# Optimization experiments

Measured on AMD Instinct MI355X. Metric: run time of the kernel, lower is better.

The kernel has to match this reference:

```python
import math
import jax, jax.numpy as jnp
import numpy as np

N_HEADS, INPUT_DIM, EMBED_DIM = 8, 512, 512
KEY_DIM = EMBED_DIM // N_HEADS  # 64, val_dim == key_dim
BATCH, N = 4, 2048


def setup_inputs() -> dict:
    key = jax.random.key(0)
    ks = jax.random.split(key, 6)
    def unif(k, shape):
        stdv = 1.0 / math.sqrt(shape[-1])
        return jax.random.uniform(k, shape, jnp.float32, -stdv, stdv)
    q = jax.random.normal(ks[0], (BATCH, N, INPUT_DIM), jnp.float32)
    mask = jax.random.randint(ks[1], (BATCH, N, N), 0, 2, jnp.int32)
    W_query = unif(ks[2], (N_HEADS, INPUT_DIM, KEY_DIM))
    W_key = unif(ks[3], (N_HEADS, INPUT_DIM, KEY_DIM))
    W_val = unif(ks[4], (N_HEADS, INPUT_DIM, KEY_DIM))
    W_out = unif(ks[5], (N_HEADS, KEY_DIM, EMBED_DIM))
    return {"q": q, "mask": mask, "W_query": W_query, "W_key": W_key,
            "W_val": W_val, "W_out": W_out}


def reference(q, mask, W_query, W_key, W_val, W_out):
    # Self-attention: k is None, v is None -> k = q, v = q (module forward_).
    norm = 1.0 / math.sqrt(KEY_DIM)
    m = mask.astype(bool)[None]  # (1, b, nq, ng) broadcast over heads
    Q = jnp.einsum('bnd,hdk->hbnk', q, W_query)  # (h, b, nq, dk)
    K = jnp.einsum('bnd,hdk->hbnk', q, W_key)    # (h, b, ng, dk)
    V = jnp.einsum('bnd,hdv->hbnv', q, W_val)    # (h, b, ng, dv)
    scores = norm * jnp.einsum('hbqk,hbgk->hbqg', Q, K)  # (h, b, nq, ng)
    scores = jnp.where(m, -jnp.inf, scores)
    attn = jax.nn.softmax(scores, axis=-1)
    attn = jnp.where(m, 0.0, attn)  # zero out masked (also kills NaN rows)
    heads = jnp.einsum('hbqg,hbgv->hbqv', attn, V)
    out = jnp.einsum('hbqv,hve->bqe', heads, W_out)  # (b, nq, embed)
    return out
```

## Files before the change

### kernel.cpp

```cpp
#include <hip/hip_runtime.h>
#include <hip/hip_bf16.h>
#include <stdint.h>

using bf16 = __hip_bfloat16;
typedef __attribute__((ext_vector_type(8))) short short8;
typedef __attribute__((ext_vector_type(4))) short short4b;
typedef __attribute__((ext_vector_type(4))) float f32x4;
typedef __attribute__((ext_vector_type(4))) unsigned int u32x4;

#if __has_builtin(__builtin_amdgcn_exp2f)
#define EXP2(x) __builtin_amdgcn_exp2f(x)
#else
#define EXP2(x) exp2f(x)
#endif

__device__ __forceinline__ short8 load8(const bf16* p) {
  return *reinterpret_cast<const short8*>(p);
}
__device__ __forceinline__ short f2b(float f) {
  return __builtin_bit_cast(short, __float2bfloat16(f));
}
__device__ __forceinline__ unsigned int pk2(float a, float b) {
  return (unsigned int)(unsigned short)f2b(a) |
         ((unsigned int)(unsigned short)f2b(b) << 16);
}
__device__ __forceinline__ void asy16(const bf16* g, bf16* l) {
  __builtin_amdgcn_global_load_lds(
      (const __attribute__((address_space(1))) void*)g,
      (__attribute__((address_space(3))) void*)l, 16, 0, 0);
}


__global__ void k_prep(const float4* __restrict__ x, ushort4* __restrict__ xb,
                       const float* __restrict__ Wq, const float* __restrict__ Wk,
                       const float* __restrict__ Wv, const float* __restrict__ Wo,
                       bf16* __restrict__ Wcat, bf16* __restrict__ Wot,
                       const int4* __restrict__ m4,
                       unsigned long long* __restrict__ bits) {
  int blk = blockIdx.x;
  const int tid = threadIdx.x;
  if (blk < 4096) {
    int i = blk * 256 + tid;
    float4 v = x[i];
    ushort4 o;
    o.x = (unsigned short)f2b(v.x);
    o.y = (unsigned short)f2b(v.y);
    o.z = (unsigned short)f2b(v.z);
    o.w = (unsigned short)f2b(v.w);
    xb[i] = o;
  } else if (blk < 4352) {
    int t = blk - 4096;
    __shared__ float T[64][65];
    if (t < 192) {
      int which = t >> 6;
      int h = (t >> 3) & 7, dt = t & 7;
      const float* W = (which == 0) ? Wq : ((which == 1) ? Wk : Wv);
#pragma unroll
      for (int p = 0; p < 4; ++p) {
        int row = p * 16 + (tid >> 4);
        float4 v = *(const float4*)(W + (size_t)(h * 512 + dt * 64 + row) * 64 +
                                    (tid & 15) * 4);
        T[row][(tid & 15) * 4 + 0] = v.x;
        T[row][(tid & 15) * 4 + 1] = v.y;
        T[row][(tid & 15) * 4 + 2] = v.z;
        T[row][(tid & 15) * 4 + 3] = v.w;
      }
      __syncthreads();
      float scale = (which == 0) ? 0.18033688011112042f : 1.0f;
      int jj = tid >> 2, i0 = (tid & 3) * 16;
#pragma unroll
      for (int q = 0; q < 2; ++q) {
        short8 o;
#pragma unroll
        for (int e = 0; e < 8; ++e) o[e] = f2b(T[i0 + q * 8 + e][jj] * scale);
        *(short8*)(Wcat + (size_t)(which * 512 + h * 64 + jj) * 512 + dt * 64 +
                   i0 + q * 8) = o;
      }
    } else {
      int t2 = t - 192;
      int h = t2 >> 3, et = t2 & 7;
#pragma unroll
      for (int p = 0; p < 4; ++p) {
        int row = p * 16 + (tid >> 4);
        float4 v = *(const float4*)(Wo + (size_t)(h * 64 + row) * 512 + et * 64 +
                                    (tid & 15) * 4);
        T[row][(tid & 15) * 4 + 0] = v.x;
        T[row][(tid & 15) * 4 + 1] = v.y;
        T[row][(tid & 15) * 4 + 2] = v.z;
        T[row][(tid & 15) * 4 + 3] = v.w;
      }
      __syncthreads();
      int jj = tid >> 2, i0 = (tid & 3) * 16;
#pragma unroll
      for (int q = 0; q < 2; ++q) {
        short8 o;
#pragma unroll
        for (int e = 0; e < 8; ++e) o[e] = f2b(T[i0 + q * 8 + e][jj]);
        *(short8*)(Wot + (size_t)(et * 64 + jj) * 512 + h * 64 + i0 + q * 8) = o;
      }
    }
  } else {
    int i = (blk - 4352) * 256 + tid;
    int4 v = m4[i];
    unsigned int nib = (unsigned)(v.x != 0) | ((unsigned)(v.y != 0) << 1) |
                       ((unsigned)(v.z != 0) << 2) | ((unsigned)(v.w != 0) << 3);
    unsigned long long w = (unsigned long long)nib << (4 * (tid & 15));
    w |= __shfl_xor(w, 1);
    w |= __shfl_xor(w, 2);
    w |= __shfl_xor(w, 4);
    w |= __shfl_xor(w, 8);
    if ((tid & 15) == 0) bits[i >> 4] = w;
  }
}

__device__ __forceinline__ void gemm128(const bf16* __restrict__ A,
                                        const bf16* __restrict__ Bt,
                                        bf16* As, bf16* Bs,
                                        int rowBase, int colBase,
                                        f32x4 acc[4][4]) {
  const int tid = threadIdx.x;
  const int lane = tid & 63, w = tid >> 6;
  const int g = lane >> 4, r = lane & 15;

  auto stage = [&](int buf, int s) {
#pragma unroll
    for (int p = 0; p < 2; ++p) {
      int c = p * 256 + tid;
      int row = c >> 2, gr = c & 3, sg = gr ^ (row & 3);
      asy16(A + (size_t)(rowBase + row) * 512 + s * 32 + sg * 8,
            As + buf * 4096 + c * 8);
    }
#pragma unroll
    for (int p = 0; p < 2; ++p) {
      int c = p * 256 + tid;
      int row = c >> 2, gr = c & 3, sg = gr ^ (row & 3);
      asy16(Bt + (size_t)(colBase + row) * 512 + s * 32 + sg * 8,
            Bs + buf * 4096 + c * 8);
    }
  };

  stage(0, 0);
  int buf = 0;
  const int rbl = (w >> 1) * 64, cbl = (w & 1) * 64;
  for (int s = 0; s < 16; ++s) {
    __syncthreads();
    if (s < 15) stage(buf ^ 1, s + 1);
    const bf16* a0 = As + buf * 4096;
    const bf16* b0 = Bs + buf * 4096;
    short8 af[4], bfr[4];
#pragma unroll
    for (int mt = 0; mt < 4; ++mt) {
      int row = rbl + mt * 16 + r;
      af[mt] = load8(a0 + (row * 4 + (g ^ (row & 3))) * 8);
    }
#pragma unroll
    for (int nt = 0; nt < 4; ++nt) {
      int col = cbl + nt * 16 + r;
      bfr[nt] = load8(b0 + (col * 4 + (g ^ (col & 3))) * 8);
    }
#pragma unroll
    for (int mt = 0; mt < 4; ++mt)
#pragma unroll
      for (int nt = 0; nt < 4; ++nt)
        acc[mt][nt] = __builtin_amdgcn_mfma_f32_16x16x32_bf16(
            af[mt], bfr[nt], acc[mt][nt], 0, 0, 0);
    buf ^= 1;
  }
}

__global__ __launch_bounds__(256, 3) void k_proj_qkv(
    const bf16* __restrict__ Xb, const bf16* __restrict__ Wcat,
    bf16* __restrict__ Qb, bf16* __restrict__ Kp, bf16* __restrict__ Vp) {
  __shared__ __align__(16) bf16 As[2 * 4096];
  __shared__ __align__(16) bf16 Bs[2 * 4096];
  int rowBase = blockIdx.x * 128, colBase = blockIdx.y * 128;
  f32x4 acc[4][4] = {};
  gemm128(Xb, Wcat, As, Bs, rowBase, colBase, acc);
  const int lane = threadIdx.x & 63, w = threadIdx.x >> 6;
  const int g = lane >> 4, r = lane & 15;
#pragma unroll
  for (int mt = 0; mt < 4; ++mt) {
    int row0 = rowBase + (w >> 1) * 64 + mt * 16 + 4 * g;
    int b = row0 >> 11, n0 = row0 & 2047;
    int kt = n0 >> 6;
#pragma unroll
    for (int nt = 0; nt < 4; ++nt) {
      int col = colBase + (w & 1) * 64 + nt * 16 + r;
      if (col < 512) {
        int hh = col >> 6, dk = col & 63;
        bf16* p0 = Qb + ((size_t)(b * 8 + hh) * 2048 + n0) * 64 + dk;
#pragma unroll
        for (int rr = 0; rr < 4; ++rr)
          p0[rr * 64] = __float2bfloat16(acc[mt][nt][rr]);
      } else if (col < 1024) {
        int hh = (col >> 6) & 7, dk = col & 63;
        int half = dk >> 5, gk = (dk >> 3) & 3, jj = dk & 7;
        int kr = n0 & 63;
        int kc = kr >> 4, r0 = kr & 15;
        bf16* base = Kp + (size_t)(b * 8 + hh) * 131072 + (size_t)kt * 4096 +
                     ((kc * 2 + half) * 4 + gk) * 128 + jj;
#pragma unroll
        for (int rr = 0; rr < 4; ++rr)
          base[(r0 + rr) * 8] = __float2bfloat16(acc[mt][nt][rr]);
      } else {
        int hdv = col - 1024;
        int hh = hdv >> 6, dv = hdv & 63;
        int dvs = dv >> 4, rv = dv & 15;
        int kcol0 = n0 & 63;
        int half = kcol0 >> 5, gv = (kcol0 >> 2) & 3;
        int j0 = ((kcol0 >> 4) & 1) * 4;
        short4b pkv;
#pragma unroll
        for (int rr = 0; rr < 4; ++rr) pkv[rr] = f2b(acc[mt][nt][rr]);
        *reinterpret_cast<short4b*>(
            Vp + (size_t)(b * 8 + hh) * 131072 + (size_t)kt * 4096 +
            (((half * 4 + dvs) * 4 + gv) * 16 + rv) * 8 + j0) = pkv;
      }
    }
  }
}

__global__ __launch_bounds__(256, 2) void k_proj_out(
    const bf16* __restrict__ O, const bf16* __restrict__ Wot,
    float* __restrict__ out) {
  __shared__ __align__(16) bf16 As[2 * 4096];
  __shared__ __align__(16) bf16 Bs[2 * 4096];
  int rowBase = blockIdx.x * 128, colBase = blockIdx.y * 128;
  f32x4 acc[4][4] = {};
  gemm128(O, Wot, As, Bs, rowBase, colBase, acc);
  const int lane = threadIdx.x & 63, w = threadIdx.x >> 6;
  const int g = lane >> 4, r = lane & 15;
#pragma unroll
  for (int mt = 0; mt < 4; ++mt) {
    int row0 = rowBase + (w >> 1) * 64 + mt * 16 + 4 * g;
#pragma unroll
    for (int nt = 0; nt < 4; ++nt) {
      int col = colBase + (w & 1) * 64 + nt * 16 + r;
#pragma unroll
      for (int rr = 0; rr < 4; ++rr)
        out[(size_t)(row0 + rr) * 512 + col] = acc[mt][nt][rr];
    }
  }
}

__global__ __launch_bounds__(256, 2) void k_attn(const bf16* __restrict__ Q,
    const bf16* __restrict__ K, const bf16* __restrict__ V,
    const unsigned long long* __restrict__ MB, bf16* __restrict__ O) {
  const int blin = blockIdx.x;
  const int j = blin >> 3;
  const int bh = (blin & 7) * 4 + (j >> 4);
  const int qt = j & 15;
  const int b = bh >> 3, h = bh & 7;
  const int tid = threadIdx.x;
  const int lane = tid & 63;
  const int wave = tid >> 6;
  const int g = lane >> 4, r = lane & 15;
  const int qbase = qt * 128 + wave * 32;

  __shared__ __align__(16) bf16 Kl[3][4096];
  __shared__ __align__(16) bf16 Vl[3][4096];

  const bf16* Kp = K + (size_t)bh * 131072;
  const bf16* Vp = V + (size_t)bh * 131072;

  short8 qf[2][2];
#pragma unroll
  for (int s = 0; s < 2; ++s) {
    const bf16* Qp = Q + ((size_t)bh * 2048 + qbase + s * 16 + r) * 64;
    qf[s][0] = load8(Qp + g * 8);
    qf[s][1] = load8(Qp + 32 + g * 8);
  }
  const unsigned long long* Mp0 = MB + ((size_t)b * 2048 + qbase + r) * 32;
  const unsigned long long* Mp1 = MB + ((size_t)b * 2048 + qbase + 16 + r) * 32;

  short8 ones;
#pragma unroll
  for (int i = 0; i < 8; ++i) ones[i] = (short)0x3F80;

  f32x4 acc[2][4] = {};
  f32x4 acc_l[2] = {};

  auto stage = [&](int buf, int kt) {
    const bf16* Kg = Kp + (size_t)kt * 4096;
    const bf16* Vg = Vp + (size_t)kt * 4096;
#pragma unroll
    for (int p = 0; p < 2; ++p) {
      int c = p * 256 + tid;
      asy16(Kg + c * 8, &Kl[buf][0] + c * 8);
    }
#pragma unroll
    for (int p = 0; p < 2; ++p) {
      int c = p * 256 + tid;
      asy16(Vg + c * 8, &Vl[buf][0] + c * 8);
    }
  };

  auto qk = [&](const bf16* kl, f32x4 stl[4][2]) {
#pragma unroll
    for (int kc = 0; kc < 4; ++kc) {
      short8 kf0 = load8(kl + ((kc * 2 + 0) * 4 + g) * 128 + r * 8);
      short8 kf1 = load8(kl + ((kc * 2 + 1) * 4 + g) * 128 + r * 8);
      f32x4 z0 = {};
      z0 = __builtin_amdgcn_mfma_f32_16x16x32_bf16(kf0, qf[0][0], z0, 0, 0, 0);
      stl[kc][0] = __builtin_amdgcn_mfma_f32_16x16x32_bf16(kf1, qf[0][1], z0, 0, 0, 0);
      f32x4 z1 = {};
      z1 = __builtin_amdgcn_mfma_f32_16x16x32_bf16(kf0, qf[1][0], z1, 0, 0, 0);
      stl[kc][1] = __builtin_amdgcn_mfma_f32_16x16x32_bf16(kf1, qf[1][1], z1, 0, 0, 0);
    }
  };

  stage(0, 0);
  stage(1, 1);
  unsigned long long mw0c = Mp0[0], mw1c = Mp1[0];
  __syncthreads();
  f32x4 st_cur[4][2];
  qk(&Kl[0][0], st_cur);

  int b_cur = 0, b_nxt = 1, b_st = 2;

  for (int kt = 0; kt < 32; ++kt) {
    __syncthreads();
    if (kt < 30) stage(b_st, kt + 2);
    unsigned long long mw0n = 0, mw1n = 0;
    if (kt < 31) { mw0n = Mp0[kt + 1]; mw1n = Mp1[kt + 1]; }

    f32x4 stn[4][2];
    if (kt < 31) qk(&Kl[b_nxt][0], stn);

    short8 pa[2][2];
#pragma unroll
    for (int s = 0; s < 2; ++s) {
      unsigned long long mw = s ? mw1c : mw0c;
      unsigned ml = (unsigned)mw >> (4 * g);
      unsigned mh = (unsigned)(mw >> 32) >> (4 * g);
      float p[16];
#pragma unroll
      for (int kc = 0; kc < 4; ++kc)
#pragma unroll
        for (int rr = 0; rr < 4; ++rr) {
          float e = EXP2(st_cur[kc][s][rr]);
          unsigned wsel = (kc & 2) ? mh : ml;
          bool bad = (wsel >> (((kc & 1) << 4) + rr)) & 1u;
          p[kc * 4 + rr] = bad ? 0.f : e;
        }
      u32x4 q0, q1;
#pragma unroll
      for (int i2 = 0; i2 < 4; ++i2) {
        q0[i2] = pk2(p[2 * i2], p[2 * i2 + 1]);
        q1[i2] = pk2(p[8 + 2 * i2], p[8 + 2 * i2 + 1]);
      }
      pa[s][0] = __builtin_bit_cast(short8, q0);
      pa[s][1] = __builtin_bit_cast(short8, q1);
      acc_l[s] = __builtin_amdgcn_mfma_f32_16x16x32_bf16(pa[s][0], ones, acc_l[s], 0, 0, 0);
      acc_l[s] = __builtin_amdgcn_mfma_f32_16x16x32_bf16(pa[s][1], ones, acc_l[s], 0, 0, 0);
    }

    const bf16* vl = &Vl[b_cur][0];
#pragma unroll
    for (int dvs = 0; dvs < 4; ++dvs) {
      short8 vb0 = load8(vl + ((0 * 4 + dvs) * 4 + g) * 128 + r * 8);
      short8 vb1 = load8(vl + ((1 * 4 + dvs) * 4 + g) * 128 + r * 8);
#pragma unroll
      for (int s = 0; s < 2; ++s) {
        acc[s][dvs] = __builtin_amdgcn_mfma_f32_16x16x32_bf16(pa[s][0], vb0, acc[s][dvs], 0, 0, 0);
        acc[s][dvs] = __builtin_amdgcn_mfma_f32_16x16x32_bf16(pa[s][1], vb1, acc[s][dvs], 0, 0, 0);
      }
    }

#pragma unroll
    for (int kc = 0; kc < 4; ++kc) {
      st_cur[kc][0] = stn[kc][0];
      st_cur[kc][1] = stn[kc][1];
    }
    mw0c = mw0n;
    mw1c = mw1n;
    int t = b_cur; b_cur = b_nxt; b_nxt = b_st; b_st = t;
  }

#pragma unroll
  for (int s = 0; s < 2; ++s) {
    float inv[4];
#pragma unroll
    for (int rr = 0; rr < 4; ++rr)
      inv[rr] = (acc_l[s][rr] > 0.f) ? 1.f / acc_l[s][rr] : 0.f;
    bf16* Op = O + ((size_t)b * 2048 + qbase + s * 16 + 4 * g) * 512 + h * 64;
#pragma unroll
    for (int dvs = 0; dvs < 4; ++dvs)
#pragma unroll
      for (int rr = 0; rr < 4; ++rr)
        Op[rr * 512 + dvs * 16 + r] = __float2bfloat16(acc[s][dvs][rr] * inv[rr]);
  }
}


extern "C" void kernel_launch(void* const* d_in, const int* in_sizes, int n_in,
                              void* d_out, int out_size, void* d_ws, size_t ws_size,
                              hipStream_t stream) {
  const float* q    = (const float*)d_in[0];
  const int*   mask = (const int*)d_in[1];
  const float* Wq   = (const float*)d_in[2];
  const float* Wk   = (const float*)d_in[3];
  const float* Wv   = (const float*)d_in[4];
  const float* Wo   = (const float*)d_in[5];
  float* out = (float*)d_out;

  char* ws = (char*)d_ws;
  const size_t MB1 = 1024 * 1024;
  bf16* Xb   = (bf16*)(ws + 0);
  bf16* Qb   = (bf16*)(ws + 8 * MB1);
  bf16* Kpm  = (bf16*)(ws + 16 * MB1);
  bf16* Vpm  = (bf16*)(ws + 24 * MB1);
  bf16* Ob   = (bf16*)(ws + 32 * MB1);
  unsigned long long* Mbits = (unsigned long long*)(ws + 40 * MB1);
  bf16* Wcat = (bf16*)(ws + 42 * MB1);
  bf16* Wot  = (bf16*)(ws + 42 * MB1 + 1536 * 512 * 2);

  k_prep<<<20736, 256, 0, stream>>>((const float4*)q, (ushort4*)Xb,
                                    Wq, Wk, Wv, Wo, Wcat, Wot,
                                    (const int4*)mask, Mbits);
  k_proj_qkv<<<dim3(64, 12), 256, 0, stream>>>(Xb, Wcat, Qb, Kpm, Vpm);
  k_attn<<<512, 256, 0, stream>>>(Qb, Kpm, Vpm, Mbits, Ob);
  k_proj_out<<<dim3(64, 4), 256, 0, stream>>>(Ob, Wot, out);
}
```

Before: 214.5 us.

## Use 8 waves of 16 query rows per attention block instead of 4x32

```diff
diff --git a/kernel.cpp b/kernel.cpp
--- a/kernel.cpp
+++ b/kernel.cpp
@@ -243,7 +243,7 @@
   }
 }
 
-__global__ __launch_bounds__(256, 2) void k_attn(const bf16* __restrict__ Q,
+__global__ __launch_bounds__(512, 4) void k_attn(const bf16* __restrict__ Q,
     const bf16* __restrict__ K, const bf16* __restrict__ V,
     const unsigned long long* __restrict__ MB, bf16* __restrict__ O) {
   const int blin = blockIdx.x;
@@ -255,7 +255,7 @@
   const int lane = tid & 63;
   const int wave = tid >> 6;
   const int g = lane >> 4, r = lane & 15;
-  const int qbase = qt * 128 + wave * 32;
+  const int qbase = qt * 128 + wave * 16;
 
   __shared__ __align__(16) bf16 Kl[3][4096];
   __shared__ __align__(16) bf16 Vl[3][4096];
@@ -263,57 +263,44 @@
   const bf16* Kp = K + (size_t)bh * 131072;
   const bf16* Vp = V + (size_t)bh * 131072;
 
-  short8 qf[2][2];
-#pragma unroll
-  for (int s = 0; s < 2; ++s) {
-    const bf16* Qp = Q + ((size_t)bh * 2048 + qbase + s * 16 + r) * 64;
-    qf[s][0] = load8(Qp + g * 8);
-    qf[s][1] = load8(Qp + 32 + g * 8);
-  }
-  const unsigned long long* Mp0 = MB + ((size_t)b * 2048 + qbase + r) * 32;
-  const unsigned long long* Mp1 = MB + ((size_t)b * 2048 + qbase + 16 + r) * 32;
+  short8 qf0, qf1;
+  {
+    const bf16* Qp = Q + ((size_t)bh * 2048 + qbase + r) * 64;
+    qf0 = load8(Qp + g * 8);
+    qf1 = load8(Qp + 32 + g * 8);
+  }
+  const unsigned long long* Mp = MB + ((size_t)b * 2048 + qbase + r) * 32;
 
   short8 ones;
 #pragma unroll
   for (int i = 0; i < 8; ++i) ones[i] = (short)0x3F80;
 
-  f32x4 acc[2][4] = {};
-  f32x4 acc_l[2] = {};
+  f32x4 acc[4] = {};
+  f32x4 acc_l = {};
 
   auto stage = [&](int buf, int kt) {
     const bf16* Kg = Kp + (size_t)kt * 4096;
     const bf16* Vg = Vp + (size_t)kt * 4096;
-#pragma unroll
-    for (int p = 0; p < 2; ++p) {
-      int c = p * 256 + tid;
-      asy16(Kg + c * 8, &Kl[buf][0] + c * 8);
-    }
-#pragma unroll
-    for (int p = 0; p < 2; ++p) {
-      int c = p * 256 + tid;
-      asy16(Vg + c * 8, &Vl[buf][0] + c * 8);
-    }
+    asy16(Kg + tid * 8, &Kl[buf][0] + tid * 8);
+    asy16(Vg + tid * 8, &Vl[buf][0] + tid * 8);
   };
 
-  auto qk = [&](const bf16* kl, f32x4 stl[4][2]) {
+  auto qk = [&](const bf16* kl, f32x4 stl[4]) {
 #pragma unroll
     for (int kc = 0; kc < 4; ++kc) {
       short8 kf0 = load8(kl + ((kc * 2 + 0) * 4 + g) * 128 + r * 8);
       short8 kf1 = load8(kl + ((kc * 2 + 1) * 4 + g) * 128 + r * 8);
-      f32x4 z0 = {};
-      z0 = __builtin_amdgcn_mfma_f32_16x16x32_bf16(kf0, qf[0][0], z0, 0, 0, 0);
-      stl[kc][0] = __builtin_amdgcn_mfma_f32_16x16x32_bf16(kf1, qf[0][1], z0, 0, 0, 0);
-      f32x4 z1 = {};
-      z1 = __builtin_amdgcn_mfma_f32_16x16x32_bf16(kf0, qf[1][0], z1, 0, 0, 0);
-      stl[kc][1] = __builtin_amdgcn_mfma_f32_16x16x32_bf16(kf1, qf[1][1], z1, 0, 0, 0);
+      f32x4 z = {};
+      z = __builtin_amdgcn_mfma_f32_16x16x32_bf16(kf0, qf0, z, 0, 0, 0);
+      stl[kc] = __builtin_amdgcn_mfma_f32_16x16x32_bf16(kf1, qf1, z, 0, 0, 0);
     }
   };
 
   stage(0, 0);
   stage(1, 1);
-  unsigned long long mw0c = Mp0[0], mw1c = Mp1[0];
+  unsigned long long mwc = Mp[0];
   __syncthreads();
-  f32x4 st_cur[4][2];
+  f32x4 st_cur[4];
   qk(&Kl[0][0], st_cur);
 
   int b_cur = 0, b_nxt = 1, b_st = 2;
@@ -321,75 +308,60 @@
   for (int kt = 0; kt < 32; ++kt) {
     __syncthreads();
     if (kt < 30) stage(b_st, kt + 2);
-    unsigned long long mw0n = 0, mw1n = 0;
-    if (kt < 31) { mw0n = Mp0[kt + 1]; mw1n = Mp1[kt + 1]; }
-
-    f32x4 stn[4][2];
+    unsigned long long mwn = 0;
+    if (kt < 31) mwn = Mp[kt + 1];
+
+    f32x4 stn[4];
     if (kt < 31) qk(&Kl[b_nxt][0], stn);
 
-    short8 pa[2][2];
-#pragma unroll
-    for (int s = 0; s < 2; ++s) {
-      unsigned long long mw = s ? mw1c : mw0c;
-      unsigned ml = (unsigned)mw >> (4 * g);
-      unsigned mh = (unsigned)(mw >> 32) >> (4 * g);
-      float p[16];
-#pragma unroll
-      for (int kc = 0; kc < 4; ++kc)
-#pragma unroll
-        for (int rr = 0; rr < 4; ++rr) {
-          float e = EXP2(st_cur[kc][s][rr]);
-          unsigned wsel = (kc & 2) ? mh : ml;
-          bool bad = (wsel >> (((kc & 1) << 4) + rr)) & 1u;
-          p[kc * 4 + rr] = bad ? 0.f : e;
-        }
-      u32x4 q0, q1;
-#pragma unroll
-      for (int i2 = 0; i2 < 4; ++i2) {
-        q0[i2] = pk2(p[2 * i2], p[2 * i2 + 1]);
-        q1[i2] = pk2(p[8 + 2 * i2], p[8 + 2 * i2 + 1]);
-      }
-      pa[s][0] = __builtin_bit_cast(short8, q0);
-      pa[s][1] = __builtin_bit_cast(short8, q1);
-      acc_l[s] = __builtin_amdgcn_mfma_f32_16x16x32_bf16(pa[s][0], ones, acc_l[s], 0, 0, 0);
-      acc_l[s] = __builtin_amdgcn_mfma_f32_16x16x32_bf16(pa[s][1], ones, acc_l[s], 0, 0, 0);
-    }
+    unsigned ml = (unsigned)mwc >> (4 * g);
+    unsigned mh = (unsigned)(mwc >> 32) >> (4 * g);
+    float p[16];
+#pragma unroll
+    for (int kc = 0; kc < 4; ++kc)
+#pragma unroll
+      for (int rr = 0; rr < 4; ++rr) {
+        float e = EXP2(st_cur[kc][rr]);
+        unsigned wsel = (kc & 2) ? mh : ml;
+        bool bad = (wsel >> (((kc & 1) << 4) + rr)) & 1u;
+        p[kc * 4 + rr] = bad ? 0.f : e;
+      }
+    u32x4 q0, q1;
+#pragma unroll
+    for (int i2 = 0; i2 < 4; ++i2) {
+      q0[i2] = pk2(p[2 * i2], p[2 * i2 + 1]);
+      q1[i2] = pk2(p[8 + 2 * i2], p[8 + 2 * i2 + 1]);
+    }
+    short8 pa0 = __builtin_bit_cast(short8, q0);
+    short8 pa1 = __builtin_bit_cast(short8, q1);
+    acc_l = __builtin_amdgcn_mfma_f32_16x16x32_bf16(pa0, ones, acc_l, 0, 0, 0);
+    acc_l = __builtin_amdgcn_mfma_f32_16x16x32_bf16(pa1, ones, acc_l, 0, 0, 0);
 
     const bf16* vl = &Vl[b_cur][0];
 #pragma unroll
     for (int dvs = 0; dvs < 4; ++dvs) {
       short8 vb0 = load8(vl + ((0 * 4 + dvs) * 4 + g) * 128 + r * 8);
       short8 vb1 = load8(vl + ((1 * 4 + dvs) * 4 + g) * 128 + r * 8);
-#pragma unroll
-      for (int s = 0; s < 2; ++s) {
-        acc[s][dvs] = __builtin_amdgcn_mfma_f32_16x16x32_bf16(pa[s][0], vb0, acc[s][dvs], 0, 0, 0);
-        acc[s][dvs] = __builtin_amdgcn_mfma_f32_16x16x32_bf16(pa[s][1], vb1, acc[s][dvs], 0, 0, 0);
-      }
-    }
-
-#pragma unroll
-    for (int kc = 0; kc < 4; ++kc) {
-      st_cur[kc][0] = stn[kc][0];
-      st_cur[kc][1] = stn[kc][1];
-    }
-    mw0c = mw0n;
-    mw1c = mw1n;
+      acc[dvs] = __builtin_amdgcn_mfma_f32_16x16x32_bf16(pa0, vb0, acc[dvs], 0, 0, 0);
+      acc[dvs] = __builtin_amdgcn_mfma_f32_16x16x32_bf16(pa1, vb1, acc[dvs], 0, 0, 0);
+    }
+
+#pragma unroll
+    for (int kc = 0; kc < 4; ++kc) st_cur[kc] = stn[kc];
+    mwc = mwn;
     int t = b_cur; b_cur = b_nxt; b_nxt = b_st; b_st = t;
   }
 
-#pragma unroll
-  for (int s = 0; s < 2; ++s) {
-    float inv[4];
+  float inv[4];
+#pragma unroll
+  for (int rr = 0; rr < 4; ++rr)
+    inv[rr] = (acc_l[rr] > 0.f) ? 1.f / acc_l[rr] : 0.f;
+  bf16* Op = O + ((size_t)b * 2048 + qbase + 4 * g) * 512 + h * 64;
+#pragma unroll
+  for (int dvs = 0; dvs < 4; ++dvs)
 #pragma unroll
     for (int rr = 0; rr < 4; ++rr)
-      inv[rr] = (acc_l[s][rr] > 0.f) ? 1.f / acc_l[s][rr] : 0.f;
-    bf16* Op = O + ((size_t)b * 2048 + qbase + s * 16 + 4 * g) * 512 + h * 64;
-#pragma unroll
-    for (int dvs = 0; dvs < 4; ++dvs)
-#pragma unroll
-      for (int rr = 0; rr < 4; ++rr)
-        Op[rr * 512 + dvs * 16 + r] = __float2bfloat16(acc[s][dvs][rr] * inv[rr]);
-  }
+      Op[rr * 512 + dvs * 16 + r] = __float2bfloat16(acc[dvs][rr] * inv[rr]);
 }
 
 
@@ -419,6 +391,6 @@
                                     Wq, Wk, Wv, Wo, Wcat, Wot,
                                     (const int4*)mask, Mbits);
   k_proj_qkv<<<dim3(64, 12), 256, 0, stream>>>(Xb, Wcat, Qb, Kpm, Vpm);
-  k_attn<<<512, 256, 0, stream>>>(Qb, Kpm, Vpm, Mbits, Ob);
+  k_attn<<<512, 512, 0, stream>>>(Qb, Kpm, Vpm, Mbits, Ob);
   k_proj_out<<<dim3(64, 4), 256, 0, stream>>>(Ob, Wot, out);
 }
```

Result: faster. 203.9 us (-5.0%).
